# Kernel tuning notes

Measured on AMD Instinct MI355X. Metric: run time of the kernel, lower is better.

The kernel has to match this reference:

```python
import jax, jax.numpy as jnp
import numpy as np

EMBED = 256; HEADS = 8; LEVELS = 4; POINTS = 4; HID = 1024
HD = EMBED // HEADS
SHAPES = [(100, 100), (50, 50), (25, 25), (13, 13)]
STARTS = [0]
for _h, _w in SHAPES[:-1]:
    STARTS.append(STARTS[-1] + _h * _w)
TOTAL = sum(h * w for h, w in SHAPES)
BS = 2
EPS = 1e-5


def _ln(x, g, b):
    m = x.mean(-1, keepdims=True)
    v = ((x - m) ** 2).mean(-1, keepdims=True)
    return (x - m) / jnp.sqrt(v + EPS) * g + b


def _msda(query, value, ref, norm_wh, params):
    W_value, b_value, W_off, b_off, W_attn, b_attn, W_out, b_out = params
    bs, T, _ = query.shape
    v = (value @ W_value + b_value).reshape(bs, T, HEADS, HD)
    v = jnp.moveaxis(v, 2, 1)  # [bs, H, T, hd]
    off = (query @ W_off + b_off).reshape(bs, T, HEADS, LEVELS, POINTS, 2)
    aw = (query @ W_attn + b_attn).reshape(bs, T, HEADS, LEVELS * POINTS)
    aw = jax.nn.softmax(aw, axis=-1).reshape(bs, T, HEADS, LEVELS, POINTS)
    aw = jnp.moveaxis(aw, 2, 1)  # [bs, H, T, L, P]
    # sampling locations in [0,1] coords: ref + offset / (W_l, H_l)
    loc = ref[:, :, None, :, None, :] + off / norm_wh[None, None, None, :, None, :]
    loc = jnp.moveaxis(loc, 2, 1)  # [bs, H, T, L, P, 2]
    out = jnp.zeros((bs, HEADS, T, HD), query.dtype)
    for l, (Hl, Wl) in enumerate(SHAPES):
        s = STARTS[l]
        v_l = v[:, :, s:s + Hl * Wl]  # [bs, H, HW_l, hd]
        # grid_sample(align_corners=False): pixel = loc * size - 0.5
        x = loc[:, :, :, l, :, 0] * Wl - 0.5  # [bs, H, T, P]
        y = loc[:, :, :, l, :, 1] * Hl - 0.5
        x0 = jnp.floor(x); y0 = jnp.floor(y)
        wx1 = x - x0; wy1 = y - y0
        x0i = x0.astype(jnp.int32); y0i = y0.astype(jnp.int32)

        def samp(xi, yi):
            valid = (xi >= 0) & (xi < Wl) & (yi >= 0) & (yi < Hl)
            idx = jnp.clip(yi, 0, Hl - 1) * Wl + jnp.clip(xi, 0, Wl - 1)
            idx = idx.reshape(bs, HEADS, -1)
            g = jnp.take_along_axis(v_l, idx[..., None], axis=2)
            g = g.reshape(bs, HEADS, T, POINTS, HD)
            return g * valid[..., None].astype(g.dtype)

        bil = ((1 - wy1) * (1 - wx1))[..., None] * samp(x0i, y0i) \
            + ((1 - wy1) * wx1)[..., None] * samp(x0i + 1, y0i) \
            + (wy1 * (1 - wx1))[..., None] * samp(x0i, y0i + 1) \
            + (wy1 * wx1)[..., None] * samp(x0i + 1, y0i + 1)
        out = out + (bil * aw[:, :, :, l, :, None]).sum(axis=3)
    out = jnp.moveaxis(out, 1, 2).reshape(bs, T, EMBED)
    return out @ W_out + b_out


def setup_inputs() -> dict:
    key = jax.random.key(0)
    ks = jax.random.split(key, 16)
    s = 0.02
    f32 = jnp.float32
    return {
        "src": jax.random.normal(ks[0], (BS, TOTAL, EMBED), f32),
        "pos": jax.random.normal(ks[1], (BS, TOTAL, EMBED), f32),
        "reference_points": jax.random.uniform(ks[2], (BS, TOTAL, LEVELS, 2), f32),
        "spatial_shapes": jnp.array(SHAPES, jnp.int32),
        "level_start_index": jnp.array(STARTS, jnp.int32),
        "ln1_g": jnp.ones((EMBED,), f32), "ln1_b": jnp.zeros((EMBED,), f32),
        "ln2_g": jnp.ones((EMBED,), f32), "ln2_b": jnp.zeros((EMBED,), f32),
        "W_value": jax.random.normal(ks[3], (EMBED, EMBED), f32) * s,
        "b_value": jnp.zeros((EMBED,), f32),
        "W_off": jax.random.normal(ks[4], (EMBED, HEADS * LEVELS * POINTS * 2), f32) * s,
        "b_off": jax.random.normal(ks[5], (HEADS * LEVELS * POINTS * 2,), f32) * 0.5,
        "W_attn": jax.random.normal(ks[6], (EMBED, HEADS * LEVELS * POINTS), f32) * s,
        "b_attn": jnp.zeros((HEADS * LEVELS * POINTS,), f32),
        "W_out": jax.random.normal(ks[7], (EMBED, EMBED), f32) * s,
        "b_out": jnp.zeros((EMBED,), f32),
        "W_ffn1": jax.random.normal(ks[8], (EMBED, HID), f32) * s,
        "b_ffn1": jnp.zeros((HID,), f32),
        "W_ffn2": jax.random.normal(ks[9], (HID, EMBED), f32) * s,
        "b_ffn2": jnp.zeros((EMBED,), f32),
    }


def reference(src, pos, reference_points, spatial_shapes, level_start_index,
              ln1_g, ln1_b, ln2_g, ln2_b,
              W_value, b_value, W_off, b_off, W_attn, b_attn, W_out, b_out,
              W_ffn1, b_ffn1, W_ffn2, b_ffn2):
    src_n = _ln(src, ln1_g, ln1_b)
    q = src_n + pos
    # offset normalizer is (W_l, H_l)
    norm_wh = jnp.stack([spatial_shapes[:, 1], spatial_shapes[:, 0]], -1).astype(src.dtype)
    attn = _msda(q, src_n, reference_points, norm_wh,
                 (W_value, b_value, W_off, b_off, W_attn, b_attn, W_out, b_out))
    src1 = src + attn  # dropout = identity (eval)
    src_n2 = _ln(src1, ln2_g, ln2_b)
    ffn = jax.nn.relu(src_n2 @ W_ffn1 + b_ffn1) @ W_ffn2 + b_ffn2
    return src1 + ffn
```

## Files before the change

kernel.cpp:

```cpp
#include <hip/hip_runtime.h>
#include <hip/hip_bf16.h>

#define T_TOK   13294
#define BS_     2
#define M_ROWS  (BS_ * T_TOK)
#define EMBED_  256
#define HID_    1024

typedef __attribute__((ext_vector_type(8))) short short8;
typedef __attribute__((ext_vector_type(4))) float f32x4;

__device__ __forceinline__ unsigned short f2bf(float f) {
  __hip_bfloat16 h = __float2bfloat16(f);
  return *reinterpret_cast<unsigned short*>(&h);
}
__device__ __forceinline__ float bf2f(unsigned short u) {
  unsigned int x = ((unsigned int)u) << 16;
  return __uint_as_float(x);
}

__global__ __launch_bounds__(256) void transpose_all_kernel(
    const float* __restrict__ s0, const float* __restrict__ s1,
    const float* __restrict__ s2, const float* __restrict__ s3,
    const float* __restrict__ s4, const float* __restrict__ s5,
    unsigned short* __restrict__ d0, unsigned short* __restrict__ d1,
    unsigned short* __restrict__ d2, unsigned short* __restrict__ d3,
    unsigned short* __restrict__ d4, unsigned short* __restrict__ d5) {
  __shared__ float t[32][33];
  const int bid = blockIdx.x;
  const float* S; unsigned short* D; int K, N, t0;
  if      (bid <  64) { S = s0; D = d0; K = 256;  N = 256;  t0 = 0;   }
  else if (bid < 128) { S = s1; D = d1; K = 256;  N = 256;  t0 = 64;  }
  else if (bid < 160) { S = s2; D = d2; K = 256;  N = 128;  t0 = 128; }
  else if (bid < 224) { S = s3; D = d3; K = 256;  N = 256;  t0 = 160; }
  else if (bid < 480) { S = s4; D = d4; K = 256;  N = 1024; t0 = 224; }
  else                { S = s5; D = d5; K = 1024; N = 256;  t0 = 480; }
  const int tile = bid - t0;
  const int ntx = N >> 5;
  const int k0 = (tile / ntx) * 32, n0 = (tile % ntx) * 32;
  const int tx = threadIdx.x, ty = threadIdx.y;
  #pragma unroll
  for (int i = 0; i < 32; i += 8)
    t[ty + i][tx] = S[(size_t)(k0 + ty + i) * N + n0 + tx];
  __syncthreads();
  #pragma unroll
  for (int i = 0; i < 32; i += 8)
    D[(size_t)(n0 + ty + i) * K + k0 + tx] = f2bf(t[tx][ty + i]);
}

template <bool ADDPOS>
__global__ __launch_bounds__(256) void ln4_kernel(
    const float* __restrict__ x, const float* __restrict__ pos,
    const float* __restrict__ g, const float* __restrict__ bta,
    unsigned short* __restrict__ y, unsigned short* __restrict__ q) {
  const int wave = threadIdx.x >> 6, lane = threadIdx.x & 63;
  const int r = blockIdx.x * 4 + wave;
  const size_t base = (size_t)r * 256 + lane * 4;
  const float4 v = *reinterpret_cast<const float4*>(&x[base]);

  float s = v.x + v.y + v.z + v.w;
  #pragma unroll
  for (int m = 32; m; m >>= 1) s += __shfl_xor(s, m, 64);
  const float mean = s * (1.0f / 256.0f);

  const float dx = v.x - mean, dy = v.y - mean, dz = v.z - mean, dw = v.w - mean;
  float s2 = dx * dx + dy * dy + dz * dz + dw * dw;
  #pragma unroll
  for (int m = 32; m; m >>= 1) s2 += __shfl_xor(s2, m, 64);
  const float rinv = rsqrtf(s2 * (1.0f / 256.0f) + 1e-5f);

  const float4 gg = *reinterpret_cast<const float4*>(&g[lane * 4]);
  const float4 bb = *reinterpret_cast<const float4*>(&bta[lane * 4]);
  const float o0 = dx * rinv * gg.x + bb.x;
  const float o1 = dy * rinv * gg.y + bb.y;
  const float o2 = dz * rinv * gg.z + bb.z;
  const float o3 = dw * rinv * gg.w + bb.w;
  ushort4 yo; yo.x = f2bf(o0); yo.y = f2bf(o1); yo.z = f2bf(o2); yo.w = f2bf(o3);
  *reinterpret_cast<ushort4*>(&y[base]) = yo;
  if (ADDPOS) {
    const float4 pp = *reinterpret_cast<const float4*>(&pos[base]);
    ushort4 qo;
    qo.x = f2bf(o0 + pp.x); qo.y = f2bf(o1 + pp.y);
    qo.z = f2bf(o2 + pp.z); qo.w = f2bf(o3 + pp.w);
    *reinterpret_cast<ushort4*>(&q[base]) = qo;
  }
}

__device__ __forceinline__ void stage64(
    const unsigned short* __restrict__ A, const unsigned short* __restrict__ Wt,
    unsigned short* As, unsigned short* Bs,
    int M, int K, int row0, int col0, int k0, int lane) {
  #pragma unroll
  for (int i = 0; i < 4; ++i) {
    const int chunk = i * 64 + lane;
    const int rrow = chunk >> 2;
    const int kgs = (chunk & 3) ^ ((rrow >> 1) & 3);
    int ga = row0 + rrow; if (ga >= M) ga = M - 1;
    __builtin_amdgcn_global_load_lds(
        (const __attribute__((address_space(1))) void*)(A + (size_t)ga * K + k0 + kgs * 8),
        (__attribute__((address_space(3))) void*)(As + chunk * 8), 16, 0, 0);
  }
  #pragma unroll
  for (int i = 0; i < 4; ++i) {
    const int chunk = i * 64 + lane;
    const int rrow = chunk >> 2;
    const int kgs = (chunk & 3) ^ ((rrow >> 1) & 3);
    __builtin_amdgcn_global_load_lds(
        (const __attribute__((address_space(1))) void*)(Wt + (size_t)(col0 + rrow) * K + k0 + kgs * 8),
        (__attribute__((address_space(3))) void*)(Bs + chunk * 8), 16, 0, 0);
  }
}

template <int EPI, bool OUTBF>
__device__ __forceinline__ void wgemm_core(
    const unsigned short* __restrict__ A, const unsigned short* __restrict__ Wt,
    const float* __restrict__ bias, const float* __restrict__ R,
    void* __restrict__ Cv, void* __restrict__ Cv2,
    int M, int N, int K, int row0, int col0, unsigned short* lds) {
  const int lane = threadIdx.x & 63;
  unsigned short* As = lds;
  unsigned short* Bs = lds + 64 * 32;

  f32x4 acc[4][4] = {};
  const int frow = lane & 15;
  const int fke = ((lane >> 4) ^ ((frow >> 1) & 3)) * 8;

  stage64(A, Wt, As, Bs, M, K, row0, col0, 0, lane);
  asm volatile("s_waitcnt vmcnt(0)" ::: "memory");

  for (int k0 = 0; k0 < K; k0 += 32) {
    short8 a[4], b[4];
    #pragma unroll
    for (int mi = 0; mi < 4; ++mi)
      a[mi] = *reinterpret_cast<const short8*>(&As[(mi * 16 + frow) * 32 + fke]);
    #pragma unroll
    for (int ni = 0; ni < 4; ++ni)
      b[ni] = *reinterpret_cast<const short8*>(&Bs[(ni * 16 + frow) * 32 + fke]);
    asm volatile("s_waitcnt lgkmcnt(0)" ::: "memory");
    __builtin_amdgcn_sched_barrier(0);

    if (k0 + 32 < K)
      stage64(A, Wt, As, Bs, M, K, row0, col0, k0 + 32, lane);

    #pragma unroll
    for (int mi = 0; mi < 4; ++mi)
      #pragma unroll
      for (int ni = 0; ni < 4; ++ni)
        acc[mi][ni] = __builtin_amdgcn_mfma_f32_16x16x32_bf16(b[ni], a[mi], acc[mi][ni], 0, 0, 0);

    if (k0 + 32 < K)
      asm volatile("s_waitcnt vmcnt(0)" ::: "memory");
  }

  const int lr = lane & 15;
  const int cb = (lane >> 4) * 4;
  #pragma unroll
  for (int mi = 0; mi < 4; ++mi) {
    const int grow = row0 + mi * 16 + lr;
    if (grow >= M) continue;
    #pragma unroll
    for (int ni = 0; ni < 4; ++ni) {
      const int gcol = col0 + ni * 16 + cb;
      float4 b4;
      if (EPI == 3) b4 = (gcol < 256) ? *reinterpret_cast<const float4*>(&bias[gcol])
                                      : *reinterpret_cast<const float4*>(&R[gcol - 256]);
      else          b4 = *reinterpret_cast<const float4*>(&bias[gcol]);
      float v0 = acc[mi][ni][0] + b4.x;
      float v1 = acc[mi][ni][1] + b4.y;
      float v2 = acc[mi][ni][2] + b4.z;
      float v3 = acc[mi][ni][3] + b4.w;
      if (EPI == 1) {
        v0 = fmaxf(v0, 0.f); v1 = fmaxf(v1, 0.f);
        v2 = fmaxf(v2, 0.f); v3 = fmaxf(v3, 0.f);
      }
      if (EPI == 2) {
        const float4 r4 = *reinterpret_cast<const float4*>(&R[(size_t)grow * N + gcol]);
        v0 += r4.x; v1 += r4.y; v2 += r4.z; v3 += r4.w;
        float4 o; o.x = v0; o.y = v1; o.z = v2; o.w = v3;
        *reinterpret_cast<float4*>(&((float*)Cv)[(size_t)grow * N + gcol]) = o;
      } else {
        ushort4 o;
        o.x = f2bf(v0); o.y = f2bf(v1); o.z = f2bf(v2); o.w = f2bf(v3);
        if (EPI == 3) {
          if (gcol < 256)
            *reinterpret_cast<ushort4*>(&((unsigned short*)Cv )[(size_t)grow * 256 + gcol]) = o;
          else
            *reinterpret_cast<ushort4*>(&((unsigned short*)Cv2)[(size_t)grow * 128 + gcol - 256]) = o;
        } else {
          *reinterpret_cast<ushort4*>(&((unsigned short*)Cv)[(size_t)grow * N + gcol]) = o;
        }
      }
    }
  }
}

template <int EPI, bool OUTBF>
__global__ __launch_bounds__(256) void wgemm_k(
    const unsigned short* __restrict__ A, const unsigned short* __restrict__ Wt,
    const float* __restrict__ bias, const float* __restrict__ R,
    void* __restrict__ Cv, int M, int N, int K) {
  __shared__ unsigned short lds[4 * 4096];
  const int w = threadIdx.x >> 6;
  const int nwg = gridDim.x;
  const int bid = blockIdx.x;
  const int wgid = (bid & 7) * (nwg >> 3) + (bid >> 3);
  const int tile = wgid * 4 + w;
  const int CT = N >> 6;
  const int row0 = (tile / CT) * 64;
  const int col0 = (tile % CT) * 64;
  wgemm_core<EPI, OUTBF>(A, Wt, bias, R, Cv, nullptr, M, N, K, row0, col0,
                         lds + w * 4096);
}

__global__ __launch_bounds__(256) void wproj_fused(
    const unsigned short* __restrict__ srcn, const unsigned short* __restrict__ q,
    const unsigned short* __restrict__ wt_val, const unsigned short* __restrict__ wt_offattn,
    const float* __restrict__ b_value, const float* __restrict__ b_off,
    const float* __restrict__ b_attn,
    unsigned short* __restrict__ vout, unsigned short* __restrict__ offout,
    unsigned short* __restrict__ awout, int M) {
  __shared__ unsigned short lds[4 * 4096];
  const int w = threadIdx.x >> 6;
  const int nwg = gridDim.x;
  const int bid = blockIdx.x;
  const int wgid = (bid & 7) * (nwg >> 3) + (bid >> 3);
  const int tile = wgid * 4 + w;
  if (tile < 1664) {
    const int row0 = (tile >> 2) * 64, col0 = (tile & 3) * 64;
    wgemm_core<0, true>(srcn, wt_val, b_value, nullptr, vout, nullptr,
                        M, 256, 256, row0, col0, lds + w * 4096);
  } else {
    const int t2 = tile - 1664;
    const int row0 = (t2 / 6) * 64, col0 = (t2 % 6) * 64;
    wgemm_core<3, false>(q, wt_offattn, b_off, b_attn, offout, awout,
                         M, 384, 256, row0, col0, lds + w * 4096);
  }
}

__global__ __launch_bounds__(256) void outln_kernel(
    const unsigned short* __restrict__ attn, const unsigned short* __restrict__ wt_out,
    const float* __restrict__ b_out, const float* __restrict__ src,
    const float* __restrict__ ln_g, const float* __restrict__ ln_b,
    float* __restrict__ src1, unsigned short* __restrict__ sn2, int M) {
  __shared__ unsigned short lds[4 * 4096];
  __shared__ float s_sum[64][4];
  __shared__ float s_sq[64][4];
  const int w = threadIdx.x >> 6, lane = threadIdx.x & 63;
  const int nwg = gridDim.x;
  const int bid = blockIdx.x;
  const int wgid = (bid & 7) * (nwg >> 3) + (bid >> 3);
  const int row0 = wgid * 64;
  const int col0 = w * 64;
  unsigned short* As = lds + w * 4096;
  unsigned short* Bs = As + 64 * 32;

  f32x4 acc[4][4] = {};
  const int frow = lane & 15;
  const int fke = ((lane >> 4) ^ ((frow >> 1) & 3)) * 8;

  stage64(attn, wt_out, As, Bs, M, 256, row0, col0, 0, lane);
  asm volatile("s_waitcnt vmcnt(0)" ::: "memory");
  for (int k0 = 0; k0 < 256; k0 += 32) {
    short8 a[4], b[4];
    #pragma unroll
    for (int mi = 0; mi < 4; ++mi)
      a[mi] = *reinterpret_cast<const short8*>(&As[(mi * 16 + frow) * 32 + fke]);
    #pragma unroll
    for (int ni = 0; ni < 4; ++ni)
      b[ni] = *reinterpret_cast<const short8*>(&Bs[(ni * 16 + frow) * 32 + fke]);
    asm volatile("s_waitcnt lgkmcnt(0)" ::: "memory");
    __builtin_amdgcn_sched_barrier(0);
    if (k0 + 32 < 256)
      stage64(attn, wt_out, As, Bs, M, 256, row0, col0, k0 + 32, lane);
    #pragma unroll
    for (int mi = 0; mi < 4; ++mi)
      #pragma unroll
      for (int ni = 0; ni < 4; ++ni)
        acc[mi][ni] = __builtin_amdgcn_mfma_f32_16x16x32_bf16(b[ni], a[mi], acc[mi][ni], 0, 0, 0);
    if (k0 + 32 < 256)
      asm volatile("s_waitcnt vmcnt(0)" ::: "memory");
  }

  const int lr = lane & 15;
  const int cb = (lane >> 4) * 4;
  float lsum[4], lsq[4];
  #pragma unroll
  for (int mi = 0; mi < 4; ++mi) {
    const int grow = row0 + mi * 16 + lr;
    const bool ok = grow < M;
    float rs = 0.f, rq = 0.f;
    #pragma unroll
    for (int ni = 0; ni < 4; ++ni) {
      const int gcol = col0 + ni * 16 + cb;
      const float4 b4 = *reinterpret_cast<const float4*>(&b_out[gcol]);
      float4 r4 = make_float4(0.f, 0.f, 0.f, 0.f);
      if (ok) r4 = *reinterpret_cast<const float4*>(&src[(size_t)grow * 256 + gcol]);
      float v0 = acc[mi][ni][0] + b4.x + r4.x;
      float v1 = acc[mi][ni][1] + b4.y + r4.y;
      float v2 = acc[mi][ni][2] + b4.z + r4.z;
      float v3 = acc[mi][ni][3] + b4.w + r4.w;
      acc[mi][ni][0] = v0; acc[mi][ni][1] = v1;
      acc[mi][ni][2] = v2; acc[mi][ni][3] = v3;
      if (ok) {
        float4 o; o.x = v0; o.y = v1; o.z = v2; o.w = v3;
        *reinterpret_cast<float4*>(&src1[(size_t)grow * 256 + gcol]) = o;
      }
      rs += v0 + v1 + v2 + v3;
      rq += v0 * v0 + v1 * v1 + v2 * v2 + v3 * v3;
    }
    lsum[mi] = rs; lsq[mi] = rq;
  }
  #pragma unroll
  for (int mi = 0; mi < 4; ++mi) {
    lsum[mi] += __shfl_xor(lsum[mi], 16, 64);
    lsum[mi] += __shfl_xor(lsum[mi], 32, 64);
    lsq[mi]  += __shfl_xor(lsq[mi], 16, 64);
    lsq[mi]  += __shfl_xor(lsq[mi], 32, 64);
  }
  if (lane < 16) {
    #pragma unroll
    for (int mi = 0; mi < 4; ++mi) {
      s_sum[mi * 16 + lane][w] = lsum[mi];
      s_sq[mi * 16 + lane][w] = lsq[mi];
    }
  }
  __syncthreads();
  #pragma unroll
  for (int mi = 0; mi < 4; ++mi) {
    const int lrow = mi * 16 + lr;
    const int grow = row0 + lrow;
    if (grow >= M) continue;
    const float s = s_sum[lrow][0] + s_sum[lrow][1] + s_sum[lrow][2] + s_sum[lrow][3];
    const float q = s_sq[lrow][0] + s_sq[lrow][1] + s_sq[lrow][2] + s_sq[lrow][3];
    const float mean = s * (1.0f / 256.0f);
    const float var = q * (1.0f / 256.0f) - mean * mean;
    const float rinv = rsqrtf(var + 1e-5f);
    #pragma unroll
    for (int ni = 0; ni < 4; ++ni) {
      const int gcol = col0 + ni * 16 + cb;
      const float4 g4 = *reinterpret_cast<const float4*>(&ln_g[gcol]);
      const float4 bb = *reinterpret_cast<const float4*>(&ln_b[gcol]);
      ushort4 o;
      o.x = f2bf((acc[mi][ni][0] - mean) * rinv * g4.x + bb.x);
      o.y = f2bf((acc[mi][ni][1] - mean) * rinv * g4.y + bb.y);
      o.z = f2bf((acc[mi][ni][2] - mean) * rinv * g4.z + bb.z);
      o.w = f2bf((acc[mi][ni][3] - mean) * rinv * g4.w + bb.w);
      *reinterpret_cast<ushort4*>(&sn2[(size_t)grow * 256 + gcol]) = o;
    }
  }
}

__global__ __launch_bounds__(256) void msda_kernel(
    const unsigned short* __restrict__ v, const unsigned short* __restrict__ offb,
    const unsigned short* __restrict__ awl, const float* __restrict__ ref,
    unsigned short* __restrict__ outb) {
  const int r0 = blockIdx.x * 8;
  const int tid = threadIdx.x;

  __shared__ float s_aw[8 * 128];
  __shared__ float s_ref[64];
  __shared__ float2 s_wi[64 * 66];

  if (tid < 64) {
    int rr = r0 + (tid >> 3); if (rr >= M_ROWS) rr = M_ROWS - 1;
    s_ref[tid] = ref[(size_t)rr * 8 + (tid & 7)];
  }

  {
    const int g = tid >> 2, j = tid & 3;
    const int tok = g >> 3, h = g & 7;
    int rr = r0 + tok; if (rr >= M_ROWS) rr = M_ROWS - 1;
    const uint2 u = *reinterpret_cast<const uint2*>(&awl[(size_t)rr * 128 + h * 16 + j * 4]);
    const float l0 = bf2f((unsigned short)(u.x & 0xffff));
    const float l1 = bf2f((unsigned short)(u.x >> 16));
    const float l2 = bf2f((unsigned short)(u.y & 0xffff));
    const float l3 = bf2f((unsigned short)(u.y >> 16));
    float mx = fmaxf(fmaxf(l0, l1), fmaxf(l2, l3));
    mx = fmaxf(mx, __shfl_xor(mx, 1, 64));
    mx = fmaxf(mx, __shfl_xor(mx, 2, 64));
    const float e0 = expf(l0 - mx), e1 = expf(l1 - mx);
    const float e2 = expf(l2 - mx), e3 = expf(l3 - mx);
    float ss = e0 + e1 + e2 + e3;
    ss += __shfl_xor(ss, 1, 64);
    ss += __shfl_xor(ss, 2, 64);
    const float inv = 1.0f / ss;
    float4 w4; w4.x = e0 * inv; w4.y = e1 * inv; w4.z = e2 * inv; w4.w = e3 * inv;
    *reinterpret_cast<float4*>(&s_aw[g * 16 + j * 4]) = w4;
  }
  __syncthreads();

  const int HH[4] = {100, 50, 25, 13};
  const int WW[4] = {100, 50, 25, 13};
  const int SS[4] = {0, 10000, 12500, 13125};

  {
    const int pi0 = tid * 4;
    const int tok = pi0 >> 7, h = (pi0 >> 4) & 7;
    const int g = pi0 >> 4;
    const int pt0 = pi0 & 15;
    const int l = pt0 >> 2;
    int rr = r0 + tok; if (rr >= M_ROWS) rr = M_ROWS - 1;
    const float Wl = (float)WW[l], Hl = (float)HH[l];
    const float rx = s_ref[tok * 8 + l * 2], ry = s_ref[tok * 8 + l * 2 + 1];
    const uint4 uoff = *reinterpret_cast<const uint4*>(&offb[(size_t)rr * 256 + h * 32 + pt0 * 2]);
    const float4 aw4 = *reinterpret_cast<const float4*>(&s_aw[g * 16 + pt0]);
    const unsigned int uo[4] = {uoff.x, uoff.y, uoff.z, uoff.w};
    const float awv[4] = {aw4.x, aw4.y, aw4.z, aw4.w};
    #pragma unroll
    for (int p = 0; p < 4; ++p) {
      const float ox = bf2f((unsigned short)(uo[p] & 0xffff));
      const float oy = bf2f((unsigned short)(uo[p] >> 16));
      const float x = rx * Wl + ox - 0.5f;
      const float y = ry * Hl + oy - 0.5f;
      const float x0f = floorf(x), y0f = floorf(y);
      const int x0 = (int)x0f, y0 = (int)y0f;
      const float wx1 = x - x0f, wy1 = y - y0f;
      const float wx0 = 1.f - wx1, wy0 = 1.f - wy1;
      const float aw = awv[p];
      #pragma unroll
      for (int c = 0; c < 4; ++c) {
        const int xx = x0 + (c & 1), yy = y0 + (c >> 1);
        const bool valid = (xx >= 0) & (xx < WW[l]) & (yy >= 0) & (yy < HH[l]);
        const int xc = min(max(xx, 0), WW[l] - 1);
        const int yc = min(max(yy, 0), HH[l] - 1);
        float wgt = aw * ((c & 1) ? wx1 : wx0) * ((c >> 1) ? wy1 : wy0);
        wgt = valid ? wgt : 0.f;
        const int idxb = (SS[l] + yc * WW[l] + xc) * 512;
        s_wi[g * 66 + (pt0 + p) * 4 + c] = make_float2(wgt, __int_as_float(idxb));
      }
    }
  }
  __syncthreads();

  const int tok = tid >> 5;
  const int h = (tid >> 2) & 7;
  const int d8 = tid & 3;
  const int r = r0 + tok;
  const int rc = (r < M_ROWS) ? r : M_ROWS - 1;
  const int b = rc / T_TOK;
  const char* vb = (const char*)(v + (size_t)b * T_TOK * 256 + h * 32 + d8 * 8);
  const int e0 = (tok * 8 + h) * 66;

  float a0 = 0.f, a1 = 0.f, a2 = 0.f, a3 = 0.f;
  float a4 = 0.f, a5 = 0.f, a6 = 0.f, a7 = 0.f;
  #pragma unroll 8
  for (int j = 0; j < 64; ++j) {
    const float2 wi = s_wi[e0 + j];
    const float wgt = wi.x;
    const int idxb = __float_as_int(wi.y);
    const uint4 u = *reinterpret_cast<const uint4*>(vb + idxb);
    a0 = fmaf(wgt, bf2f((unsigned short)(u.x & 0xffff)), a0);
    a1 = fmaf(wgt, bf2f((unsigned short)(u.x >> 16)), a1);
    a2 = fmaf(wgt, bf2f((unsigned short)(u.y & 0xffff)), a2);
    a3 = fmaf(wgt, bf2f((unsigned short)(u.y >> 16)), a3);
    a4 = fmaf(wgt, bf2f((unsigned short)(u.z & 0xffff)), a4);
    a5 = fmaf(wgt, bf2f((unsigned short)(u.z >> 16)), a5);
    a6 = fmaf(wgt, bf2f((unsigned short)(u.w & 0xffff)), a6);
    a7 = fmaf(wgt, bf2f((unsigned short)(u.w >> 16)), a7);
  }
  if (r < M_ROWS) {
    uint4 o;
    o.x = ((unsigned int)f2bf(a0)) | ((unsigned int)f2bf(a1) << 16);
    o.y = ((unsigned int)f2bf(a2)) | ((unsigned int)f2bf(a3) << 16);
    o.z = ((unsigned int)f2bf(a4)) | ((unsigned int)f2bf(a5) << 16);
    o.w = ((unsigned int)f2bf(a6)) | ((unsigned int)f2bf(a7) << 16);
    *reinterpret_cast<uint4*>(&outb[(size_t)r * 256 + h * 32 + d8 * 8]) = o;
  }
}

extern "C" void kernel_launch(void* const* d_in, const int* in_sizes, int n_in,
                              void* d_out, int out_size, void* d_ws, size_t ws_size,
                              hipStream_t stream) {
  const float* src     = (const float*)d_in[0];
  const float* pos     = (const float*)d_in[1];
  const float* ref     = (const float*)d_in[2];
  const float* ln1_g   = (const float*)d_in[5];
  const float* ln1_b   = (const float*)d_in[6];
  const float* ln2_g   = (const float*)d_in[7];
  const float* ln2_b   = (const float*)d_in[8];
  const float* W_value = (const float*)d_in[9];
  const float* b_value = (const float*)d_in[10];
  const float* W_off   = (const float*)d_in[11];
  const float* b_off   = (const float*)d_in[12];
  const float* W_attn  = (const float*)d_in[13];
  const float* b_attn  = (const float*)d_in[14];
  const float* W_out   = (const float*)d_in[15];
  const float* b_out   = (const float*)d_in[16];
  const float* W_ffn1  = (const float*)d_in[17];
  const float* b_ffn1  = (const float*)d_in[18];
  const float* W_ffn2  = (const float*)d_in[19];
  const float* b_ffn2  = (const float*)d_in[20];
  float* out = (float*)d_out;

  const int M = M_ROWS;
  const size_t n256 = (size_t)M * 256;

  unsigned short* src_n_bf = (unsigned short*)d_ws;
  unsigned short* q_bf     = src_n_bf + n256;
  unsigned short* v_bf     = q_bf + n256;
  unsigned short* attn_bf  = v_bf + n256;
  unsigned short* sn2_bf   = attn_bf + n256;
  unsigned short* hid_bf   = sn2_bf + n256;
  unsigned short* offb     = hid_bf + (size_t)M * 1024;
  unsigned short* awbuf    = offb + n256;
  float* src1 = (float*)(awbuf + (size_t)M * 128);
  unsigned short* wt_val     = (unsigned short*)(src1 + n256);
  unsigned short* wt_offattn = wt_val + 256 * 256;
  unsigned short* wt_out     = wt_offattn + 384 * 256;
  unsigned short* wt_ffn1    = wt_out + 256 * 256;
  unsigned short* wt_ffn2    = wt_ffn1 + 1024 * 256;

  transpose_all_kernel<<<736, dim3(32, 8), 0, stream>>>(
      W_value, W_off, W_attn, W_out, W_ffn1, W_ffn2,
      wt_val, wt_offattn, wt_offattn + 256 * 256, wt_out, wt_ffn1, wt_ffn2);

  ln4_kernel<true><<<M / 4, 256, 0, stream>>>(src, pos, ln1_g, ln1_b, src_n_bf, q_bf);

  wproj_fused<<<1040, 256, 0, stream>>>(
      src_n_bf, q_bf, wt_val, wt_offattn, b_value, b_off, b_attn,
      v_bf, offb, awbuf, M);

  msda_kernel<<<(M + 7) / 8, 256, 0, stream>>>(v_bf, offb, awbuf, ref, attn_bf);

  outln_kernel<<<416, 256, 0, stream>>>(attn_bf, wt_out, b_out, src,
                                        ln2_g, ln2_b, src1, sn2_bf, M);

  wgemm_k<1, true ><<<1664, 256, 0, stream>>>(sn2_bf, wt_ffn1, b_ffn1, nullptr,
                                              hid_bf, M, 1024, 256);
  wgemm_k<2, false><<<416, 256, 0, stream>>>(hid_bf, wt_ffn2, b_ffn2, src1,
                                             out, M, 256, 1024);
}
```

Before: 200.1 us.

## Merge weight transpose with first LayerNorm, template K, add occupancy hints

Folds the weight-transpose kernel and the first LayerNorm kernel into one launch, with block ranges picking the role, which saves one kernel launch and lets the two run concurrently. Makes the GEMM K dimension a template parameter so the k-loops can be fully unrolled with constant addressing. Adds __launch_bounds__(256,3) to the GEMM kernels to cap register use for higher occupancy. Full unrolling may enlarge code and raise register pressure, and the occupancy cap could cause spills.

```diff
diff --git a/kernel.cpp b/kernel.cpp
--- a/kernel.cpp
+++ b/kernel.cpp
@@ -19,55 +19,55 @@
   return __uint_as_float(x);
 }
 
-__global__ __launch_bounds__(256) void transpose_all_kernel(
+__global__ __launch_bounds__(256) void prep_kernel(
     const float* __restrict__ s0, const float* __restrict__ s1,
     const float* __restrict__ s2, const float* __restrict__ s3,
     const float* __restrict__ s4, const float* __restrict__ s5,
     unsigned short* __restrict__ d0, unsigned short* __restrict__ d1,
     unsigned short* __restrict__ d2, unsigned short* __restrict__ d3,
-    unsigned short* __restrict__ d4, unsigned short* __restrict__ d5) {
-  __shared__ float t[32][33];
-  const int bid = blockIdx.x;
-  const float* S; unsigned short* D; int K, N, t0;
-  if      (bid <  64) { S = s0; D = d0; K = 256;  N = 256;  t0 = 0;   }
-  else if (bid < 128) { S = s1; D = d1; K = 256;  N = 256;  t0 = 64;  }
-  else if (bid < 160) { S = s2; D = d2; K = 256;  N = 128;  t0 = 128; }
-  else if (bid < 224) { S = s3; D = d3; K = 256;  N = 256;  t0 = 160; }
-  else if (bid < 480) { S = s4; D = d4; K = 256;  N = 1024; t0 = 224; }
-  else                { S = s5; D = d5; K = 1024; N = 256;  t0 = 480; }
-  const int tile = bid - t0;
-  const int ntx = N >> 5;
-  const int k0 = (tile / ntx) * 32, n0 = (tile % ntx) * 32;
-  const int tx = threadIdx.x, ty = threadIdx.y;
-  #pragma unroll
-  for (int i = 0; i < 32; i += 8)
-    t[ty + i][tx] = S[(size_t)(k0 + ty + i) * N + n0 + tx];
-  __syncthreads();
-  #pragma unroll
-  for (int i = 0; i < 32; i += 8)
-    D[(size_t)(n0 + ty + i) * K + k0 + tx] = f2bf(t[tx][ty + i]);
-}
-
-template <bool ADDPOS>
-__global__ __launch_bounds__(256) void ln4_kernel(
+    unsigned short* __restrict__ d4, unsigned short* __restrict__ d5,
     const float* __restrict__ x, const float* __restrict__ pos,
     const float* __restrict__ g, const float* __restrict__ bta,
     unsigned short* __restrict__ y, unsigned short* __restrict__ q) {
+  const int bid = blockIdx.x;
+  if (bid < 736) {
+    __shared__ float t[32][33];
+    const float* S; unsigned short* D; int K, N, t0;
+    if      (bid <  64) { S = s0; D = d0; K = 256;  N = 256;  t0 = 0;   }
+    else if (bid < 128) { S = s1; D = d1; K = 256;  N = 256;  t0 = 64;  }
+    else if (bid < 160) { S = s2; D = d2; K = 256;  N = 128;  t0 = 128; }
+    else if (bid < 224) { S = s3; D = d3; K = 256;  N = 256;  t0 = 160; }
+    else if (bid < 480) { S = s4; D = d4; K = 256;  N = 1024; t0 = 224; }
+    else                { S = s5; D = d5; K = 1024; N = 256;  t0 = 480; }
+    const int tile = bid - t0;
+    const int ntx = N >> 5;
+    const int k0 = (tile / ntx) * 32, n0 = (tile % ntx) * 32;
+    const int tx = threadIdx.x & 31, ty = threadIdx.x >> 5;
+    #pragma unroll
+    for (int i = 0; i < 32; i += 8)
+      t[ty + i][tx] = S[(size_t)(k0 + ty + i) * N + n0 + tx];
+    __syncthreads();
+    #pragma unroll
+    for (int i = 0; i < 32; i += 8)
+      D[(size_t)(n0 + ty + i) * K + k0 + tx] = f2bf(t[tx][ty + i]);
+    return;
+  }
   const int wave = threadIdx.x >> 6, lane = threadIdx.x & 63;
-  const int r = blockIdx.x * 4 + wave;
+  const int r = (bid - 736) * 4 + wave;
+  if (r >= M_ROWS) return;
   const size_t base = (size_t)r * 256 + lane * 4;
   const float4 v = *reinterpret_cast<const float4*>(&x[base]);
 
-  float s = v.x + v.y + v.z + v.w;
-  #pragma unroll
-  for (int m = 32; m; m >>= 1) s += __shfl_xor(s, m, 64);
-  const float mean = s * (1.0f / 256.0f);
+  float lsum = v.x + v.y + v.z + v.w;
+  #pragma unroll
+  for (int m = 32; m; m >>= 1) lsum += __shfl_xor(lsum, m, 64);
+  const float mean = lsum * (1.0f / 256.0f);
 
   const float dx = v.x - mean, dy = v.y - mean, dz = v.z - mean, dw = v.w - mean;
-  float s2 = dx * dx + dy * dy + dz * dz + dw * dw;
-  #pragma unroll
-  for (int m = 32; m; m >>= 1) s2 += __shfl_xor(s2, m, 64);
-  const float rinv = rsqrtf(s2 * (1.0f / 256.0f) + 1e-5f);
+  float lsq = dx * dx + dy * dy + dz * dz + dw * dw;
+  #pragma unroll
+  for (int m = 32; m; m >>= 1) lsq += __shfl_xor(lsq, m, 64);
+  const float rinv = rsqrtf(lsq * (1.0f / 256.0f) + 1e-5f);
 
   const float4 gg = *reinterpret_cast<const float4*>(&g[lane * 4]);
   const float4 bb = *reinterpret_cast<const float4*>(&bta[lane * 4]);
@@ -77,19 +77,18 @@
   const float o3 = dw * rinv * gg.w + bb.w;
   ushort4 yo; yo.x = f2bf(o0); yo.y = f2bf(o1); yo.z = f2bf(o2); yo.w = f2bf(o3);
   *reinterpret_cast<ushort4*>(&y[base]) = yo;
-  if (ADDPOS) {
-    const float4 pp = *reinterpret_cast<const float4*>(&pos[base]);
-    ushort4 qo;
-    qo.x = f2bf(o0 + pp.x); qo.y = f2bf(o1 + pp.y);
-    qo.z = f2bf(o2 + pp.z); qo.w = f2bf(o3 + pp.w);
-    *reinterpret_cast<ushort4*>(&q[base]) = qo;
-  }
-}
-
+  const float4 pp = *reinterpret_cast<const float4*>(&pos[base]);
+  ushort4 qo;
+  qo.x = f2bf(o0 + pp.x); qo.y = f2bf(o1 + pp.y);
+  qo.z = f2bf(o2 + pp.z); qo.w = f2bf(o3 + pp.w);
+  *reinterpret_cast<ushort4*>(&q[base]) = qo;
+}
+
+template <int K>
 __device__ __forceinline__ void stage64(
     const unsigned short* __restrict__ A, const unsigned short* __restrict__ Wt,
     unsigned short* As, unsigned short* Bs,
-    int M, int K, int row0, int col0, int k0, int lane) {
+    int M, int row0, int col0, int k0, int lane) {
   #pragma unroll
   for (int i = 0; i < 4; ++i) {
     const int chunk = i * 64 + lane;
@@ -111,12 +110,12 @@
   }
 }
 
-template <int EPI, bool OUTBF>
+template <int EPI, bool OUTBF, int K>
 __device__ __forceinline__ void wgemm_core(
     const unsigned short* __restrict__ A, const unsigned short* __restrict__ Wt,
     const float* __restrict__ bias, const float* __restrict__ R,
     void* __restrict__ Cv, void* __restrict__ Cv2,
-    int M, int N, int K, int row0, int col0, unsigned short* lds) {
+    int M, int N, int row0, int col0, unsigned short* lds) {
   const int lane = threadIdx.x & 63;
   unsigned short* As = lds;
   unsigned short* Bs = lds + 64 * 32;
@@ -125,9 +124,10 @@
   const int frow = lane & 15;
   const int fke = ((lane >> 4) ^ ((frow >> 1) & 3)) * 8;
 
-  stage64(A, Wt, As, Bs, M, K, row0, col0, 0, lane);
+  stage64<K>(A, Wt, As, Bs, M, row0, col0, 0, lane);
   asm volatile("s_waitcnt vmcnt(0)" ::: "memory");
 
+  #pragma unroll
   for (int k0 = 0; k0 < K; k0 += 32) {
     short8 a[4], b[4];
     #pragma unroll
@@ -140,7 +140,7 @@
     __builtin_amdgcn_sched_barrier(0);
 
     if (k0 + 32 < K)
-      stage64(A, Wt, As, Bs, M, K, row0, col0, k0 + 32, lane);
+      stage64<K>(A, Wt, As, Bs, M, row0, col0, k0 + 32, lane);
 
     #pragma unroll
     for (int mi = 0; mi < 4; ++mi)
@@ -194,11 +194,11 @@
   }
 }
 
-template <int EPI, bool OUTBF>
-__global__ __launch_bounds__(256) void wgemm_k(
+template <int EPI, bool OUTBF, int K>
+__global__ __launch_bounds__(256, 3) void wgemm_k(
     const unsigned short* __restrict__ A, const unsigned short* __restrict__ Wt,
     const float* __restrict__ bias, const float* __restrict__ R,
-    void* __restrict__ Cv, int M, int N, int K) {
+    void* __restrict__ Cv, int M, int N) {
   __shared__ unsigned short lds[4 * 4096];
   const int w = threadIdx.x >> 6;
   const int nwg = gridDim.x;
@@ -208,11 +208,11 @@
   const int CT = N >> 6;
   const int row0 = (tile / CT) * 64;
   const int col0 = (tile % CT) * 64;
-  wgemm_core<EPI, OUTBF>(A, Wt, bias, R, Cv, nullptr, M, N, K, row0, col0,
-                         lds + w * 4096);
-}
-
-__global__ __launch_bounds__(256) void wproj_fused(
+  wgemm_core<EPI, OUTBF, K>(A, Wt, bias, R, Cv, nullptr, M, N, row0, col0,
+                            lds + w * 4096);
+}
+
+__global__ __launch_bounds__(256, 3) void wproj_fused(
     const unsigned short* __restrict__ srcn, const unsigned short* __restrict__ q,
     const unsigned short* __restrict__ wt_val, const unsigned short* __restrict__ wt_offattn,
     const float* __restrict__ b_value, const float* __restrict__ b_off,
@@ -227,17 +227,17 @@
   const int tile = wgid * 4 + w;
   if (tile < 1664) {
     const int row0 = (tile >> 2) * 64, col0 = (tile & 3) * 64;
-    wgemm_core<0, true>(srcn, wt_val, b_value, nullptr, vout, nullptr,
-                        M, 256, 256, row0, col0, lds + w * 4096);
+    wgemm_core<0, true, 256>(srcn, wt_val, b_value, nullptr, vout, nullptr,
+                             M, 256, row0, col0, lds + w * 4096);
   } else {
     const int t2 = tile - 1664;
     const int row0 = (t2 / 6) * 64, col0 = (t2 % 6) * 64;
-    wgemm_core<3, false>(q, wt_offattn, b_off, b_attn, offout, awout,
-                         M, 384, 256, row0, col0, lds + w * 4096);
-  }
-}
-
-__global__ __launch_bounds__(256) void outln_kernel(
+    wgemm_core<3, false, 256>(q, wt_offattn, b_off, b_attn, offout, awout,
+                              M, 384, row0, col0, lds + w * 4096);
+  }
+}
+
+__global__ __launch_bounds__(256, 3) void outln_kernel(
     const unsigned short* __restrict__ attn, const unsigned short* __restrict__ wt_out,
     const float* __restrict__ b_out, const float* __restrict__ src,
     const float* __restrict__ ln_g, const float* __restrict__ ln_b,
@@ -258,8 +258,9 @@
   const int frow = lane & 15;
   const int fke = ((lane >> 4) ^ ((frow >> 1) & 3)) * 8;
 
-  stage64(attn, wt_out, As, Bs, M, 256, row0, col0, 0, lane);
+  stage64<256>(attn, wt_out, As, Bs, M, row0, col0, 0, lane);
   asm volatile("s_waitcnt vmcnt(0)" ::: "memory");
+  #pragma unroll
   for (int k0 = 0; k0 < 256; k0 += 32) {
     short8 a[4], b[4];
     #pragma unroll
@@ -271,7 +272,7 @@
     asm volatile("s_waitcnt lgkmcnt(0)" ::: "memory");
     __builtin_amdgcn_sched_barrier(0);
     if (k0 + 32 < 256)
-      stage64(attn, wt_out, As, Bs, M, 256, row0, col0, k0 + 32, lane);
+      stage64<256>(attn, wt_out, As, Bs, M, row0, col0, k0 + 32, lane);
     #pragma unroll
     for (int mi = 0; mi < 4; ++mi)
       #pragma unroll
@@ -330,10 +331,10 @@
     const int lrow = mi * 16 + lr;
     const int grow = row0 + lrow;
     if (grow >= M) continue;
-    const float s = s_sum[lrow][0] + s_sum[lrow][1] + s_sum[lrow][2] + s_sum[lrow][3];
-    const float q = s_sq[lrow][0] + s_sq[lrow][1] + s_sq[lrow][2] + s_sq[lrow][3];
-    const float mean = s * (1.0f / 256.0f);
-    const float var = q * (1.0f / 256.0f) - mean * mean;
+    const float ssum = s_sum[lrow][0] + s_sum[lrow][1] + s_sum[lrow][2] + s_sum[lrow][3];
+    const float ssq = s_sq[lrow][0] + s_sq[lrow][1] + s_sq[lrow][2] + s_sq[lrow][3];
+    const float mean = ssum * (1.0f / 256.0f);
+    const float var = ssq * (1.0f / 256.0f) - mean * mean;
     const float rinv = rsqrtf(var + 1e-5f);
     #pragma unroll
     for (int ni = 0; ni < 4; ++ni) {
@@ -510,11 +511,10 @@
   unsigned short* wt_ffn1    = wt_out + 256 * 256;
   unsigned short* wt_ffn2    = wt_ffn1 + 1024 * 256;
 
-  transpose_all_kernel<<<736, dim3(32, 8), 0, stream>>>(
+  prep_kernel<<<736 + (M + 3) / 4, 256, 0, stream>>>(
       W_value, W_off, W_attn, W_out, W_ffn1, W_ffn2,
-      wt_val, wt_offattn, wt_offattn + 256 * 256, wt_out, wt_ffn1, wt_ffn2);
-
-  ln4_kernel<true><<<M / 4, 256, 0, stream>>>(src, pos, ln1_g, ln1_b, src_n_bf, q_bf);
+      wt_val, wt_offattn, wt_offattn + 256 * 256, wt_out, wt_ffn1, wt_ffn2,
+      src, pos, ln1_g, ln1_b, src_n_bf, q_bf);
 
   wproj_fused<<<1040, 256, 0, stream>>>(
       src_n_bf, q_bf, wt_val, wt_offattn, b_value, b_off, b_attn,
@@ -525,8 +525,8 @@
   outln_kernel<<<416, 256, 0, stream>>>(attn_bf, wt_out, b_out, src,
                                         ln2_g, ln2_b, src1, sn2_bf, M);
 
-  wgemm_k<1, true ><<<1664, 256, 0, stream>>>(sn2_bf, wt_ffn1, b_ffn1, nullptr,
-                                              hid_bf, M, 1024, 256);
-  wgemm_k<2, false><<<416, 256, 0, stream>>>(hid_bf, wt_ffn2, b_ffn2, src1,
-                                             out, M, 256, 1024);
-}
+  wgemm_k<1, true, 256 ><<<1664, 256, 0, stream>>>(sn2_bf, wt_ffn1, b_ffn1, nullptr,
+                                                   hid_bf, M, 1024);
+  wgemm_k<2, false, 1024><<<416, 256, 0, stream>>>(hid_bf, wt_ffn2, b_ffn2, src1,
+                                                   out, M, 256);
+}
```

New measurement: 188.2 us, median of 2. -6.0%, faster.
